# Kernel tuning notes

Hardware: AMD Instinct MI355X
Metric: run time of the kernel (lower is better)

Reference implementation:

```python
import jax, jax.numpy as jnp
import numpy as np

BUCKET_BINS = np.array([0, 1, 2, 3, 4, 5, 7, 8, 15, 16, 31, 32, 63, 64], dtype=np.int32)
MAX_WINDOW = 8  # args.span_maximum_length


def _span_index_table(L):
    # Static enumeration of all spans of width 1..MAX_WINDOW (stride-1 unfold).
    starts, ends = [], []
    for w in range(1, min(L, MAX_WINDOW) + 1):
        s = np.arange(0, L - w + 1)
        starts.append(s)
        ends.append(s + w)
    return (np.concatenate(starts).astype(np.int32),
            np.concatenate(ends).astype(np.int32))


def _bucket(width):
    # index of last bin with width >= bin value
    return jnp.searchsorted(jnp.asarray(BUCKET_BINS), width, side='right') - 1


def _fnn(h, W1, b1, W2, b2, W3, b3):
    # Linear->ReLU->(Dropout: eval identity)->Linear->ReLU->Linear->Softmax
    h = jax.nn.relu(h @ W1 + b1)
    h = jax.nn.relu(h @ W2 + b2)
    return jax.nn.softmax(h @ W3 + b3, axis=-1)


def setup_inputs() -> dict:
    key = jax.random.key(0)
    ks = jax.random.split(key, 16)
    B, L, D = 8, 256, 768
    H, WD, DD = 1024, 25, 25
    span_dim = 2 * D + WD          # 1561
    pair_dim = 2 * span_dim + DD   # 3147
    f = jnp.float32

    def g(k, shape, scale):
        return jax.random.normal(k, shape, dtype=f) * scale

    return {
        'x': g(ks[0], (B, L, D), 1.0),
        'width_emb': g(ks[1], (len(BUCKET_BINS), WD), 0.02),
        'dist_emb': g(ks[2], (len(BUCKET_BINS), DD), 0.02),
        'Ws1': g(ks[3], (span_dim, H), 0.02), 'bs1': jnp.zeros((H,), f),
        'Ws2': g(ks[4], (H, H), 0.02), 'bs2': jnp.zeros((H,), f),
        'Ws3': g(ks[5], (H, 3), 0.02), 'bs3': jnp.zeros((3,), f),
        'Wp1': g(ks[6], (pair_dim, H), 0.02), 'bp1': jnp.zeros((H,), f),
        'Wp2': g(ks[7], (H, H), 0.02), 'bp2': jnp.zeros((H,), f),
        'Wp3': g(ks[8], (H, 4), 0.02), 'bp3': jnp.zeros((4,), f),
        'nz': 64,
    }


def reference(x, width_emb, dist_emb, Ws1, bs1, Ws2, bs2, Ws3, bs3,
              Wp1, bp1, Wp2, bp2, Wp3, bp3, nz):
    B, L, D = x.shape
    starts_np, ends_np = _span_index_table(L)
    starts = jnp.asarray(starts_np)
    ends = jnp.asarray(ends_np)

    # ---- SpanRepresentation: [start token, end token, width bucket emb] ----
    w_emb = width_emb[_bucket(ends - starts)]                     # [S, WD]
    spans = jnp.concatenate([
        x[:, starts_np, :],                                       # [B,S,D]
        x[:, ends_np - 1, :],                                     # [B,S,D]
        jnp.broadcast_to(w_emb, (B,) + w_emb.shape),              # [B,S,WD]
    ], axis=-1)                                                   # [B,S,span_dim]

    # ---- span_fnn + PrunedTargetOpinion (top-k on aspect/opinion probs) ----
    span_prob = _fnn(spans, Ws1, bs1, Ws2, bs2, Ws3, bs3)         # [B,S,3]
    _, t_idx = jax.lax.top_k(span_prob[:, :, 1], nz)              # aspect  [B,nz]
    _, o_idx = jax.lax.top_k(span_prob[:, :, 2], nz)              # opinion [B,nz]

    # ---- PairRepresentation: all target x opinion pairs ----
    t_rep = jnp.take_along_axis(spans, t_idx[:, :, None], axis=1) # [B,nz,sd]
    o_rep = jnp.take_along_axis(spans, o_idx[:, :, None], axis=1)
    ta, tb = starts[t_idx], ends[t_idx]                           # [B,nz]
    oc, od = starts[o_idx], ends[o_idx]
    # min_distance(a,b,c,d) = min(|b-c|, |a-d|)
    dist = jnp.minimum(jnp.abs(tb[:, :, None] - oc[:, None, :]),
                       jnp.abs(ta[:, :, None] - od[:, None, :]))  # [B,nz,nz]
    d_emb = dist_emb[_bucket(dist)]                               # [B,nz,nz,DD]
    sd = spans.shape[-1]
    pairs = jnp.concatenate([
        jnp.broadcast_to(t_rep[:, :, None, :], (B, nz, nz, sd)),
        jnp.broadcast_to(o_rep[:, None, :, :], (B, nz, nz, sd)),
        d_emb,
    ], axis=-1).reshape(B, nz * nz, 2 * sd + d_emb.shape[-1])     # [B,nz^2,pair_dim]

    pair_prob = _fnn(pairs, Wp1, bp1, Wp2, bp2, Wp3, bp3)         # [B,nz^2,4]
    return span_prob, pair_prob
```

## Files before the change

kernel.cpp:

```cpp
#include <hip/hip_runtime.h>
#include <cstdint>
#include <cstddef>

#define BATCH 8
#define SEQ   256
#define DIM   768
#define NSPAN 2020
#define HID   1024
#define NZ    64

typedef unsigned short u16;
typedef unsigned int   u32;
typedef unsigned long long u64;

typedef __bf16 bf16x8 __attribute__((ext_vector_type(8)));
typedef float  f32x4  __attribute__((ext_vector_type(4)));

__device__ __forceinline__ u16 f2bf(float f) {
    union { float f; u32 u; } x; x.f = f;
    u32 r = x.u + 0x7fffu + ((x.u >> 16) & 1u);
    return (u16)(r >> 16);
}
__device__ __forceinline__ float bf2f(u16 b) {
    union { u32 u; float f; } x; x.u = ((u32)b) << 16;
    return x.f;
}
__device__ __forceinline__ void splitbf(float v, u16& h, u16& l) {
    h = f2bf(v);
    l = f2bf(v - bf2f(h));
}

__device__ __forceinline__ void gld_lds16(const void* g, void* l) {
    __builtin_amdgcn_global_load_lds(
        (const __attribute__((address_space(1))) unsigned int*)g,
        (__attribute__((address_space(3))) unsigned int*)l, 16, 0, 0);
}

__device__ __forceinline__ void span_decode(int s, int& start, int& end, int& w) {
    int off = 0;
#pragma unroll
    for (int wi = 1; wi <= 8; ++wi) {
        int cnt = SEQ - wi + 1;
        if (s < off + cnt) { w = wi; start = s - off; end = start + wi; return; }
        off += cnt;
    }
    w = 8; start = 0; end = 8;
}

__device__ __forceinline__ int dbucket(int d) {
    int b = 0;
    b += (d >= 1);  b += (d >= 2);  b += (d >= 3);  b += (d >= 4);
    b += (d >= 5);  b += (d >= 7);  b += (d >= 8);  b += (d >= 15);
    b += (d >= 16); b += (d >= 31); b += (d >= 32); b += (d >= 63);
    b += (d >= 64);
    return b;
}

__device__ __forceinline__ void xcd_map(int L, int sft, int& bx, int& by) {
    int grp = L >> (3 + sft);
    int rem = L & ((1 << (3 + sft)) - 1);
    bx = rem >> 3;
    by = (grp << 3) | (rem & 7);
}

__global__ __launch_bounds__(256) void k_prep(
    const float* __restrict__ x,  u16* __restrict__ xh,   u16* __restrict__ xl,
    const float* __restrict__ wemb, const float* __restrict__ demb,
    const float* __restrict__ bs1, const float* __restrict__ bp1,
    float* __restrict__ wtabS, float* __restrict__ wtabPt,
    float* __restrict__ wtabPo, float* __restrict__ dtab,
    const float* __restrict__ Ws1, u16* __restrict__ W1Th, u16* __restrict__ W1Tl,
    const float* __restrict__ Ws2, u16* __restrict__ W2Th, u16* __restrict__ W2Tl,
    const float* __restrict__ Wp2, u16* __restrict__ Wp2T,
    const float* __restrict__ Wp1, u16* __restrict__ Wp1T4)
{
    __shared__ float tile[32][33];
    const int bid = blockIdx.x, tid = threadIdx.x;
    if (bid < 6144) {
        int i = bid * 256 + tid;
        u16 h, l; splitbf(x[i], h, l);
        xh[i] = h; xl[i] = l;
        return;
    }
    if (bid < 6296) {
        int t = bid - 6144;
        int row = t >> 2;
        int h = (t & 3) * 256 + tid;
        const int wb[8] = {1,2,3,4,5,5,6,7};
        if (row < 8) {
            int bk = wb[row];
            float acc = bs1[h];
            for (int j = 0; j < 25; ++j) acc = fmaf(wemb[bk*25+j], Ws1[(size_t)(1536+j)*HID + h], acc);
            wtabS[row*HID + h] = acc;
        } else if (row < 16) {
            int bk = wb[row-8];
            float acc = 0.f;
            for (int j = 0; j < 25; ++j) acc = fmaf(wemb[bk*25+j], Wp1[(size_t)(1536+j)*HID + h], acc);
            wtabPt[(row-8)*HID + h] = acc;
        } else if (row < 24) {
            int bk = wb[row-16];
            float acc = 0.f;
            for (int j = 0; j < 25; ++j) acc = fmaf(wemb[bk*25+j], Wp1[(size_t)(3097+j)*HID + h], acc);
            wtabPo[(row-16)*HID + h] = acc;
        } else {
            int tt = row - 24;
            float acc = bp1[h];
            for (int j = 0; j < 25; ++j) acc = fmaf(demb[tt*25+j], Wp1[(size_t)(3122+j)*HID + h], acc);
            dtab[tt*HID + h] = acc;
        }
        return;
    }
    const int tb = bid - 6296;
    const int tr = tid >> 3;
    const int tc4 = (tid & 7) * 4;
    int job, tk, tn, blk = 0;
    if (tb < 1536)      { job = 0; tk = tb % 24; tn = tb / 24; }
    else if (tb < 2560) { job = 1; int t = tb - 1536; tk = t & 31; tn = t >> 5; }
    else if (tb < 3584) { job = 2; int t = tb - 2560; tk = t & 31; tn = t >> 5; }
    else                { job = 3; int t = tb - 3584; blk = t / 768; int r = t - blk * 768; tk = r % 24; tn = r / 24; }
    const int k0 = tk * 32, n0 = tn * 32;

    int k = k0 + tr;
    float4 v;
    if (job == 0) {
        const float* s = (n0 < 1024) ? (Ws1 + (size_t)k * HID + n0)
                                     : (Ws1 + (size_t)(768 + k) * HID + (n0 - 1024));
        v = *(const float4*)(s + tc4);
    } else if (job == 1) {
        v = *(const float4*)(Ws2 + (size_t)k * HID + n0 + tc4);
    } else if (job == 2) {
        v = *(const float4*)(Wp2 + (size_t)k * HID + n0 + tc4);
    } else {
        const int roff[4] = {0, 768, 1561, 2329};
        v = *(const float4*)(Wp1 + (size_t)(roff[blk] + k) * HID + n0 + tc4);
    }
    tile[tr][tc4+0] = v.x; tile[tr][tc4+1] = v.y;
    tile[tr][tc4+2] = v.z; tile[tr][tc4+3] = v.w;
    __syncthreads();

    int nn = n0 + tr;
    float w0 = tile[tc4+0][tr], w1 = tile[tc4+1][tr];
    float w2 = tile[tc4+2][tr], w3 = tile[tc4+3][tr];
    if (job == 0) {
        size_t d = (size_t)nn * 768 + k0 + tc4;
        u16 h0,l0,h1,l1,h2,l2,h3,l3;
        splitbf(w0,h0,l0); splitbf(w1,h1,l1); splitbf(w2,h2,l2); splitbf(w3,h3,l3);
        *(uint2*)(W1Th + d) = make_uint2((u32)h0 | ((u32)h1 << 16), (u32)h2 | ((u32)h3 << 16));
        *(uint2*)(W1Tl + d) = make_uint2((u32)l0 | ((u32)l1 << 16), (u32)l2 | ((u32)l3 << 16));
    } else if (job == 1) {
        size_t d = (size_t)nn * 1024 + k0 + tc4;
        u16 h0,l0,h1,l1,h2,l2,h3,l3;
        splitbf(w0,h0,l0); splitbf(w1,h1,l1); splitbf(w2,h2,l2); splitbf(w3,h3,l3);
        *(uint2*)(W2Th + d) = make_uint2((u32)h0 | ((u32)h1 << 16), (u32)h2 | ((u32)h3 << 16));
        *(uint2*)(W2Tl + d) = make_uint2((u32)l0 | ((u32)l1 << 16), (u32)l2 | ((u32)l3 << 16));
    } else if (job == 2) {
        size_t d = (size_t)nn * 1024 + k0 + tc4;
        *(uint2*)(Wp2T + d) = make_uint2((u32)f2bf(w0) | ((u32)f2bf(w1) << 16),
                                         (u32)f2bf(w2) | ((u32)f2bf(w3) << 16));
    } else {
        size_t d = (size_t)blk * 786432 + (size_t)nn * 768 + k0 + tc4;
        *(uint2*)(Wp1T4 + d) = make_uint2((u32)f2bf(w0) | ((u32)f2bf(w1) << 16),
                                          (u32)f2bf(w2) | ((u32)f2bf(w3) << 16));
    }
}

__global__ __launch_bounds__(256) void k_gemm3bf(
    const u16* __restrict__ Ah, const u16* __restrict__ Al, int lda,
    const u16* __restrict__ BTh, const u16* __restrict__ BTl, int ldb,
    float* __restrict__ C, int ldc,
    int M, int K, int nby, int sft)
{
    int bx, by;
    xcd_map(blockIdx.x, sft, bx, by);
    if (by >= nby) return;
    __shared__ __align__(16) u16 sm[4 * 128 * 32];
    u16* sAh = sm;
    u16* sAl = sm + 4096;
    u16* sBh = sm + 8192;
    u16* sBl = sm + 12288;
    const int tid = threadIdx.x;
    const int bm = by * 128, bn = bx * 128;
    const int wave = tid >> 6, lane = tid & 63;
    const int wr = wave >> 1, wc = wave & 1;
    const int q = lane >> 4, tl = lane & 15;

    f32x4 zero = {0.f, 0.f, 0.f, 0.f};
    f32x4 acc[4][4];
#pragma unroll
    for (int i = 0; i < 4; ++i)
#pragma unroll
        for (int j = 0; j < 4; ++j) acc[i][j] = zero;

    const int srow = lane >> 2;
    const int scol = (lane & 3) * 8;
    int ra0 = bm + wave * 32 + srow;      if (ra0 >= M) ra0 = M - 1;
    int ra1 = bm + wave * 32 + 16 + srow; if (ra1 >= M) ra1 = M - 1;
    const int rb0 = bn + wave * 32 + srow;
    const int rb1 = bn + wave * 32 + 16 + srow;
    u16* dA0 = sAh + wave * 1024;  u16* dA1 = dA0 + 512;
    u16* dL0 = sAl + wave * 1024;  u16* dL1 = dL0 + 512;
    u16* dB0 = sBh + wave * 1024;  u16* dB1 = dB0 + 512;
    u16* dC0 = sBl + wave * 1024;  u16* dC1 = dC0 + 512;
    const u16* gA0 = Ah  + (size_t)ra0 * lda + scol;
    const u16* gA1 = Ah  + (size_t)ra1 * lda + scol;
    const u16* gL0 = Al  + (size_t)ra0 * lda + scol;
    const u16* gL1 = Al  + (size_t)ra1 * lda + scol;
    const u16* gB0 = BTh + (size_t)rb0 * ldb + scol;
    const u16* gB1 = BTh + (size_t)rb1 * ldb + scol;
    const u16* gC0 = BTl + (size_t)rb0 * ldb + scol;
    const u16* gC1 = BTl + (size_t)rb1 * ldb + scol;

    for (int k0 = 0; k0 < K; k0 += 32) {
        gld_lds16(gA0 + k0, dA0);
        gld_lds16(gA1 + k0, dA1);
        gld_lds16(gL0 + k0, dL0);
        gld_lds16(gL1 + k0, dL1);
        gld_lds16(gB0 + k0, dB0);
        gld_lds16(gB1 + k0, dB1);
        gld_lds16(gC0 + k0, dC0);
        gld_lds16(gC1 + k0, dC1);
        __syncthreads();
        bf16x8 ah[4], al[4], bh[4], bl[4];
#pragma unroll
        for (int t = 0; t < 4; ++t) {
            int arow = (wr*64 + t*16 + tl) * 32 + q*8;
            int brow = (wc*64 + t*16 + tl) * 32 + q*8;
            ah[t] = *(const bf16x8*)(&sAh[arow]);
            al[t] = *(const bf16x8*)(&sAl[arow]);
            bh[t] = *(const bf16x8*)(&sBh[brow]);
            bl[t] = *(const bf16x8*)(&sBl[brow]);
        }
#pragma unroll
        for (int ti = 0; ti < 4; ++ti)
#pragma unroll
            for (int tj = 0; tj < 4; ++tj) {
                acc[ti][tj] = __builtin_amdgcn_mfma_f32_16x16x32_bf16(ah[ti], bh[tj], acc[ti][tj], 0, 0, 0);
                acc[ti][tj] = __builtin_amdgcn_mfma_f32_16x16x32_bf16(al[ti], bh[tj], acc[ti][tj], 0, 0, 0);
                acc[ti][tj] = __builtin_amdgcn_mfma_f32_16x16x32_bf16(ah[ti], bl[tj], acc[ti][tj], 0, 0, 0);
            }
        __syncthreads();
    }
#pragma unroll
    for (int ti = 0; ti < 4; ++ti) {
#pragma unroll
        for (int tj = 0; tj < 4; ++tj) {
            int gcol = bn + wc*64 + tj*16 + tl;
#pragma unroll
            for (int r = 0; r < 4; ++r) {
                int grow = bm + wr*64 + ti*16 + q*4 + r;
                if (grow >= M) continue;
                C[(size_t)grow * ldc + gcol] = acc[ti][tj][r];
            }
        }
    }
}

#define MFB __builtin_amdgcn_mfma_f32_16x16x32_bf16
#define MFROW(i, A, B) \
    acc[i][0] = MFB(A, B[0], acc[i][0], 0, 0, 0); \
    acc[i][1] = MFB(A, B[1], acc[i][1], 0, 0, 0); \
    acc[i][2] = MFB(A, B[2], acc[i][2], 0, 0, 0); \
    acc[i][3] = MFB(A, B[3], acc[i][3], 0, 0, 0);

__global__ __launch_bounds__(512, 2) void k_span_l2(
    const u16* __restrict__ Ah, const u16* __restrict__ Al,
    const u16* __restrict__ BTh, const u16* __restrict__ BTl,
    const float* __restrict__ bs2, const float* __restrict__ Ws3,
    float* __restrict__ part, int M)
{
    __shared__ __align__(16) u16 sm[65536];
    const int tid = threadIdx.x;
    const int swz = (blockIdx.x & 7) * 32 + (blockIdx.x >> 3);
    const int by = swz >> 2, bx = swz & 3;
    const int bm = by * 256, bn = bx * 256;
    const int wave = tid >> 6, lane = tid & 63;
    const int wm = wave >> 2, wn = wave & 3;
    const int tl = lane & 15, q8 = lane >> 4;

    const int sr  = lane >> 2;
    const int scs = lane & 3;
    const int scl = scs ^ ((sr >> 1) & 3);
    const u16* gsrc[8];
    u32 ldst[8];
#pragma unroll
    for (int c = 0; c < 4; ++c) {
        int arr  = 2 + (c >> 1);
        int half = c & 1;
        int sb   = wave;
        int row  = bn + half * 128 + sb * 16 + sr;
        const u16* base = (arr == 2) ? BTh : BTl;
        gsrc[c] = base + (size_t)row * HID + scl * 8;
        ldst[c] = arr * 8192 + half * 4096 + sb * 512;
    }
#pragma unroll
    for (int p = 0; p < 4; ++p) {
        int arr  = wave >> 2;
        int half = (wave >> 1) & 1;
        int sb   = 2 * p + (wave & 1);
        int row  = bm + half * 128 + sb * 16 + sr;
        if (row >= M) row = M - 1;
        const u16* base = arr ? Al : Ah;
        gsrc[4 + p] = base + (size_t)row * HID + scl * 8;
        ldst[4 + p] = arr * 8192 + half * 4096 + sb * 512;
    }
    const int cpr = q8 ^ ((tl >> 1) & 3);
    const u32 lof = (u32)(tl * 32 + cpr * 8);
    const u32 rA  = (u32)(wm * 4096) + lof;
    const u32 rB  = 16384u + (u32)((wn >> 1) * 4096 + (wn & 1) * 2048) + lof;

    f32x4 zero = {0.f, 0.f, 0.f, 0.f};
    f32x4 acc[8][4];
#pragma unroll
    for (int i = 0; i < 8; ++i)
#pragma unroll
        for (int j = 0; j < 4; ++j) acc[i][j] = zero;

#pragma unroll
    for (int c = 0; c < 8; ++c) gld_lds16(gsrc[c], sm + ldst[c]);
    asm volatile("s_waitcnt vmcnt(3)" ::: "memory");
    asm volatile("s_barrier" ::: "memory");

    bf16x8 bh[4], bl[4];
    bf16x8 aXh0, aXh1, aXl0, aXl1, aYh0, aYh1, aYl0, aYl1;
#pragma unroll
    for (int fn = 0; fn < 4; ++fn) {
        bh[fn] = *(const bf16x8*)(sm + rB + fn * 512);
        bl[fn] = *(const bf16x8*)(sm + rB + 8192 + fn * 512);
    }
    aXh0 = *(const bf16x8*)(sm + rA + 0 * 512);
    aXh1 = *(const bf16x8*)(sm + rA + 1 * 512);
    aXl0 = *(const bf16x8*)(sm + rA + 8192 + 0 * 512);
    aXl1 = *(const bf16x8*)(sm + rA + 8192 + 1 * 512);

    for (int t = 0; t < 32; ++t) {
        const u16* smr = sm + ((t & 1) ? 32768u : 0u);
        u16*       smw = sm + ((t & 1) ? 0u : 32768u);
        const int  kn  = (t + 1) * 32;
        gld_lds16(gsrc[0] + kn, smw + ldst[0]);
        gld_lds16(gsrc[1] + kn, smw + ldst[1]);
        gld_lds16(gsrc[2] + kn, smw + ldst[2]);
        asm volatile("s_waitcnt vmcnt(5)" ::: "memory");
        asm volatile("s_barrier" ::: "memory");
        __builtin_amdgcn_sched_barrier(0);
        __builtin_amdgcn_s_setprio(1);
        MFROW(0, aXh0, bh) MFROW(1, aXh1, bh)
        MFROW(0, aXl0, bh) MFROW(1, aXl1, bh)
        MFROW(0, aXh0, bl) MFROW(1, aXh1, bl)
        __builtin_amdgcn_s_setprio(0);
        __builtin_amdgcn_sched_barrier(0);
        aYh0 = *(const bf16x8*)(smr + rA + 2 * 512);
        aYh1 = *(const bf16x8*)(smr + rA + 3 * 512);
        aYl0 = *(const bf16x8*)(smr + rA + 8192 + 2 * 512);
        aYl1 = *(const bf16x8*)(smr + rA + 8192 + 3 * 512);
        gld_lds16(gsrc[3] + kn, smw + ldst[3]);
        gld_lds16(gsrc[4] + kn, smw + ldst[4]);
        asm volatile("s_waitcnt vmcnt(6)" ::: "memory");
        asm volatile("s_barrier" ::: "memory");
        __builtin_amdgcn_sched_barrier(0);
        __builtin_amdgcn_s_setprio(1);
        MFROW(2, aYh0, bh) MFROW(3, aYh1, bh)
        MFROW(2, aYl0, bh) MFROW(3, aYl1, bh)
        MFROW(2, aYh0, bl) MFROW(3, aYh1, bl)
        __builtin_amdgcn_s_setprio(0);
        __builtin_amdgcn_sched_barrier(0);
        aXh0 = *(const bf16x8*)(smr + rA + 4 * 512);
        aXh1 = *(const bf16x8*)(smr + rA + 5 * 512);
        aXl0 = *(const bf16x8*)(smr + rA + 8192 + 4 * 512);
        aXl1 = *(const bf16x8*)(smr + rA + 8192 + 5 * 512);
        gld_lds16(gsrc[5] + kn, smw + ldst[5]);
        gld_lds16(gsrc[6] + kn, smw + ldst[6]);
        asm volatile("s_waitcnt vmcnt(7)" ::: "memory");
        asm volatile("s_barrier" ::: "memory");
        __builtin_amdgcn_sched_barrier(0);
        __builtin_amdgcn_s_setprio(1);
        MFROW(4, aXh0, bh) MFROW(5, aXh1, bh)
        MFROW(4, aXl0, bh) MFROW(5, aXl1, bh)
        MFROW(4, aXh0, bl) MFROW(5, aXh1, bl)
        __builtin_amdgcn_s_setprio(0);
        __builtin_amdgcn_sched_barrier(0);
        aYh0 = *(const bf16x8*)(smr + rA + 6 * 512);
        aYh1 = *(const bf16x8*)(smr + rA + 7 * 512);
        aYl0 = *(const bf16x8*)(smr + rA + 8192 + 6 * 512);
        aYl1 = *(const bf16x8*)(smr + rA + 8192 + 7 * 512);
        gld_lds16(gsrc[7] + kn, smw + ldst[7]);
        asm volatile("s_waitcnt vmcnt(3)" ::: "memory");
        asm volatile("s_barrier" ::: "memory");
        __builtin_amdgcn_sched_barrier(0);
        __builtin_amdgcn_s_setprio(1);
        MFROW(6, aYh0, bh) MFROW(7, aYh1, bh)
        MFROW(6, aYl0, bh) MFROW(7, aYl1, bh)
        MFROW(6, aYh0, bl) MFROW(7, aYh1, bl)
        __builtin_amdgcn_s_setprio(0);
        __builtin_amdgcn_sched_barrier(0);
        aXh0 = *(const bf16x8*)(smw + rA + 0 * 512);
        aXh1 = *(const bf16x8*)(smw + rA + 1 * 512);
        aXl0 = *(const bf16x8*)(smw + rA + 8192 + 0 * 512);
        aXl1 = *(const bf16x8*)(smw + rA + 8192 + 1 * 512);
#pragma unroll
        for (int fn = 0; fn < 4; ++fn) {
            bh[fn] = *(const bf16x8*)(smw + rB + fn * 512);
            bl[fn] = *(const bf16x8*)(smw + rB + 8192 + fn * 512);
        }
        asm volatile("s_barrier" ::: "memory");
    }

    const int slot = bx * 4 + wn;
#pragma unroll
    for (int fm = 0; fm < 8; ++fm) {
#pragma unroll
        for (int r = 0; r < 4; ++r) {
            int grow = bm + wm * 128 + fm * 16 + q8 * 4 + r;
            float l0 = 0.f, l1 = 0.f, l2 = 0.f;
#pragma unroll
            for (int fn = 0; fn < 4; ++fn) {
                int gcol = bn + wn * 64 + fn * 16 + tl;
                float v = fmaxf(acc[fm][fn][r] + bs2[gcol], 0.f);
                const float* w3 = Ws3 + gcol * 3;
                l0 = fmaf(v, w3[0], l0);
                l1 = fmaf(v, w3[1], l1);
                l2 = fmaf(v, w3[2], l2);
            }
#pragma unroll
            for (int off = 8; off > 0; off >>= 1) {
                l0 += __shfl_down(l0, off, 16);
                l1 += __shfl_down(l1, off, 16);
                l2 += __shfl_down(l2, off, 16);
            }
            if (tl == 0 && grow < M) {
                float* dst = part + ((size_t)grow * 16 + slot) * 3;
                dst[0] = l0; dst[1] = l1; dst[2] = l2;
            }
        }
    }
    asm volatile("s_waitcnt vmcnt(0)" ::: "memory");
}

__global__ __launch_bounds__(256) void k_pairL1(
    const u16* __restrict__ xh, const u16* __restrict__ Wp1T4,
    float* __restrict__ TO2, const int* __restrict__ toks)
{
    __shared__ __align__(16) u16 sm[2 * 64 * 32];
    u16* sA = sm;
    u16* sB = sm + 2048;
    const int tid = threadIdx.x;
    const int bid = blockIdx.x;
    const int p = bid >> 8;
    const int bx = bid & 15, by = (bid >> 4) & 15;
    const int bm = by * 64, bn = bx * 64;
    const int wave = tid >> 6, lane = tid & 63;
    const int wr = wave >> 1, wc = wave & 1;
    const int q = lane >> 4, tl = lane & 15;
    const bool isO = bm >= 512;

    f32x4 zero = {0.f, 0.f, 0.f, 0.f};
    f32x4 acc[2][2];
#pragma unroll
    for (int i = 0; i < 2; ++i)
#pragma unroll
        for (int j = 0; j < 2; ++j) acc[i][j] = zero;

    const int srow = tid >> 2;
    const int scol = (tid & 3) * 8;
    u16* dA = sA + wave * 512;
    u16* dB = sB + wave * 512;

    int arow = toks[bm + srow + p * 1024];
    const u16* gA = xh + (size_t)arow * DIM + scol;
    const u16* gB = Wp1T4 + ((size_t)((isO ? 2 : 0) + p) * 1024 + bn + srow) * DIM + scol;
    for (int k0 = 0; k0 < DIM; k0 += 32) {
        gld_lds16(gA + k0, dA);
        gld_lds16(gB + k0, dB);
        __syncthreads();
        bf16x8 af[2], bf[2];
#pragma unroll
        for (int t = 0; t < 2; ++t) {
            af[t] = *(const bf16x8*)(&sA[(wr*32 + t*16 + tl) * 32 + q*8]);
            bf[t] = *(const bf16x8*)(&sB[(wc*32 + t*16 + tl) * 32 + q*8]);
        }
#pragma unroll
        for (int ti = 0; ti < 2; ++ti)
#pragma unroll
            for (int tj = 0; tj < 2; ++tj)
                acc[ti][tj] = __builtin_amdgcn_mfma_f32_16x16x32_bf16(af[ti], bf[tj], acc[ti][tj], 0, 0, 0);
        __syncthreads();
    }
    float* dstb = TO2 + (size_t)p * 1024 * HID;
#pragma unroll
    for (int ti = 0; ti < 2; ++ti) {
#pragma unroll
        for (int tj = 0; tj < 2; ++tj) {
            int gcol = bn + wc*32 + tj*16 + tl;
#pragma unroll
            for (int r = 0; r < 4; ++r) {
                int grow = bm + wr*32 + ti*16 + q*4 + r;
                dstb[(size_t)grow * HID + gcol] = acc[ti][tj][r];
            }
        }
    }
}

__global__ __launch_bounds__(256) void k_build_h1s(
    const float* __restrict__ XALL, const float* __restrict__ wtabS,
    u16* __restrict__ h1h, u16* __restrict__ h1l)
{
    int r = blockIdx.x;
    int b = r / NSPAN, s = r - b * NSPAN;
    int st, en, w; span_decode(s, st, en, w);
    const float4* xs = (const float4*)(XALL + (size_t)(b*SEQ + st) * 2048);
    const float4* xe = (const float4*)(XALL + (size_t)(b*SEQ + en - 1) * 2048 + 1024);
    const float4* wt = (const float4*)(wtabS + (size_t)(w-1) * HID);
    int t = threadIdx.x;
    float4 a = xs[t], bz = xe[t], c = wt[t];
    float v0 = fmaxf(a.x + bz.x + c.x, 0.f);
    float v1 = fmaxf(a.y + bz.y + c.y, 0.f);
    float v2 = fmaxf(a.z + bz.z + c.z, 0.f);
    float v3 = fmaxf(a.w + bz.w + c.w, 0.f);
    u16 h0,l0,h1,l1,h2,l2,h3,l3;
    splitbf(v0,h0,l0); splitbf(v1,h1,l1); splitbf(v2,h2,l2); splitbf(v3,h3,l3);
    size_t base = (size_t)r * HID + t * 4;
    *(uint2*)(h1h + base) = make_uint2((u32)h0 | ((u32)h1 << 16), (u32)h2 | ((u32)h3 << 16));
    *(uint2*)(h1l + base) = make_uint2((u32)l0 | ((u32)l1 << 16), (u32)l2 | ((u32)l3 << 16));
}

__global__ __launch_bounds__(1024) void k_topk(
    const float* __restrict__ partS, const float* __restrict__ bs3,
    float* __restrict__ out, int* __restrict__ t_idx, int* __restrict__ o_idx,
    int* __restrict__ toks)
{
    int b = blockIdx.x >> 1;
    int head = 1 + (blockIdx.x & 1);
    int* outp = (head == 1 ? t_idx : o_idx) + b * NZ;
    __shared__ u64 keys[2048];
    int tid = threadIdx.x;
#pragma unroll
    for (int ii = 0; ii < 2; ++ii) {
        int s = tid + ii * 1024;
        u32 fb = 0;
        if (s < NSPAN) {
            const float* p = partS + (size_t)(b * NSPAN + s) * 48;
            float s0 = bs3[0], s1 = bs3[1], s2 = bs3[2];
#pragma unroll
            for (int t = 0; t < 16; ++t) {
                s0 += p[t*3]; s1 += p[t*3+1]; s2 += p[t*3+2];
            }
            float m = fmaxf(s0, fmaxf(s1, s2));
            float e0 = expf(s0 - m), e1 = expf(s1 - m), e2 = expf(s2 - m);
            float inv = 1.f / (e0 + e1 + e2);
            float p0 = e0 * inv, p1 = e1 * inv, p2 = e2 * inv;
            float* o = out + (size_t)(b * NSPAN + s) * 3;
            o[0] = p0; o[1] = p1; o[2] = p2;
            union { float f; u32 u; } x;
            x.f = (head == 1) ? p1 : p2;
            fb = x.u;
        }
        keys[s] = ((u64)fb << 32) | (u64)(0xFFFFFFFFu - (u32)s);
    }
    __syncthreads();
    for (int k = 2; k <= 2048; k <<= 1) {
        for (int j = k >> 1; j > 0; j >>= 1) {
#pragma unroll
            for (int ii = 0; ii < 2; ++ii) {
                int i = tid + ii * 1024;
                int ixj = i ^ j;
                if (ixj > i) {
                    u64 a = keys[i], c = keys[ixj];
                    bool desc = (i & k) == 0;
                    bool wrong = desc ? (a < c) : (a > c);
                    if (wrong) { keys[i] = c; keys[ixj] = a; }
                }
            }
            __syncthreads();
        }
    }
    if (tid < NZ) {
        u64 key = keys[tid];
        int fi = (int)(0xFFFFFFFFu - (u32)(key & 0xFFFFFFFFu));
        if (fi < 0 || fi >= NSPAN) fi = 0;
        outp[tid] = fi;
        int st, en, w; span_decode(fi, st, en, w);
        int base = (head == 1 ? 0 : 512) + b * NZ + tid;
        toks[base] = b * SEQ + st;
        toks[1024 + base] = b * SEQ + en - 1;
    }
}

__global__ __launch_bounds__(256) void k_build_h1p(
    const float* __restrict__ TO2, const int* __restrict__ t_idx, const int* __restrict__ o_idx,
    const float* __restrict__ wtabPt, const float* __restrict__ wtabPo,
    const float* __restrict__ dtab, u16* __restrict__ h1p)
{
    __shared__ float Ts[8][HID];
    __shared__ float Os[4][HID];
    const int bid = blockIdx.x;
    const int b = bid >> 7;
    const int it = (bid >> 4) & 7;
    const int jt = bid & 15;
    const int i0 = it * 8, j0 = jt * 4;
    const int tid = threadIdx.x;
    const int k4 = tid * 4;
    const size_t PS = (size_t)1024 * HID;

    int tinfo[8][2];
    int oinfo[4][2];
#pragma unroll
    for (int r = 0; r < 8; ++r) {
        int i = i0 + r;
        int ts = t_idx[b*64 + i];
        int ta, tb, wt; span_decode(ts, ta, tb, wt);
        tinfo[r][0] = ta; tinfo[r][1] = tb;
        float4 t0 = *(const float4*)(TO2 + (size_t)(b*64 + i) * HID + k4);
        float4 t1 = *(const float4*)(TO2 + PS + (size_t)(b*64 + i) * HID + k4);
        float4 pp = *(const float4*)(wtabPt + (size_t)(wt-1) * HID + k4);
        Ts[r][k4+0] = t0.x + t1.x + pp.x;
        Ts[r][k4+1] = t0.y + t1.y + pp.y;
        Ts[r][k4+2] = t0.z + t1.z + pp.z;
        Ts[r][k4+3] = t0.w + t1.w + pp.w;
    }
#pragma unroll
    for (int r = 0; r < 4; ++r) {
        int j = j0 + r;
        int os = o_idx[b*64 + j];
        int oc, od, wo; span_decode(os, oc, od, wo);
        oinfo[r][0] = oc; oinfo[r][1] = od;
        float4 o0 = *(const float4*)(TO2 + (size_t)(512 + b*64 + j) * HID + k4);
        float4 o1 = *(const float4*)(TO2 + PS + (size_t)(512 + b*64 + j) * HID + k4);
        float4 qq = *(const float4*)(wtabPo + (size_t)(wo-1) * HID + k4);
        Os[r][k4+0] = o0.x + o1.x + qq.x;
        Os[r][k4+1] = o0.y + o1.y + qq.y;
        Os[r][k4+2] = o0.z + o1.z + qq.z;
        Os[r][k4+3] = o0.w + o1.w + qq.w;
    }
    __syncthreads();

#pragma unroll
    for (int ri = 0; ri < 8; ++ri) {
#pragma unroll
        for (int rj = 0; rj < 4; ++rj) {
            int ta = tinfo[ri][0], tb = tinfo[ri][1];
            int oc = oinfo[rj][0], od = oinfo[rj][1];
            int d1 = tb - oc; d1 = d1 < 0 ? -d1 : d1;
            int d2 = ta - od; d2 = d2 < 0 ? -d2 : d2;
            int dist = d1 < d2 ? d1 : d2;
            int db = dbucket(dist);
            const float4 dd = *(const float4*)(dtab + (size_t)db * HID + k4);
            float vx = fmaxf(Ts[ri][k4+0] + Os[rj][k4+0] + dd.x, 0.f);
            float vy = fmaxf(Ts[ri][k4+1] + Os[rj][k4+1] + dd.y, 0.f);
            float vz = fmaxf(Ts[ri][k4+2] + Os[rj][k4+2] + dd.z, 0.f);
            float vw = fmaxf(Ts[ri][k4+3] + Os[rj][k4+3] + dd.w, 0.f);
            u32 p0 = (u32)f2bf(vx) | ((u32)f2bf(vy) << 16);
            u32 p1 = (u32)f2bf(vz) | ((u32)f2bf(vw) << 16);
            int row = b * 4096 + (i0 + ri) * 64 + (j0 + rj);
            *(uint2*)(h1p + (size_t)row * HID + k4) = make_uint2(p0, p1);
        }
    }
}

#define MFROWP(i, A0, A1, B0, B1) \
    acc[i][0] = MFB(A0, B0[0], acc[i][0], 0, 0, 0); \
    acc[i][1] = MFB(A0, B0[1], acc[i][1], 0, 0, 0); \
    acc[i][2] = MFB(A0, B0[2], acc[i][2], 0, 0, 0); \
    acc[i][3] = MFB(A0, B0[3], acc[i][3], 0, 0, 0);

__global__ __launch_bounds__(512, 2) void k_pair_l2(
    const u16* __restrict__ Abf, const u16* __restrict__ BT,
    const float* __restrict__ bp2, const float* __restrict__ Wp3,
    float* __restrict__ part)
{
    __shared__ __align__(16) u16 sm[65536];
    const int tid = threadIdx.x;
    const int swz = (blockIdx.x & 7) * 64 + (blockIdx.x >> 3);
    const int by = swz >> 2, bx = swz & 3;
    const int bm = by * 256, bn = bx * 256;
    const int wave = tid >> 6, lane = tid & 63;
    const int wm = wave >> 2, wn = wave & 3;
    const int tl = lane & 15, q8 = lane >> 4;

    const int sr  = lane >> 2;
    const int scs = lane & 3;
    const int scl = scs ^ ((sr >> 1) & 3);
    const u16* gsrc[8];
    u32 ldst[8];
#pragma unroll
    for (int c = 0; c < 4; ++c) {
        int half = c >> 1;
        int sb   = (c & 1) * 8 + wave;
        int row  = bn + half * 128 + (sb >> 1) * 16 + sr;
        gsrc[c] = BT + (size_t)row * HID + (sb & 1) * 32 + scl * 8;
        ldst[c] = 16384 + half * 8192 + sb * 512;
    }
#pragma unroll
    for (int p = 0; p < 4; ++p) {
        int half = wave >> 2;
        int sb   = 4 * p + (wave & 3);
        int row  = bm + half * 128 + (sb >> 1) * 16 + sr;
        gsrc[4 + p] = Abf + (size_t)row * HID + (sb & 1) * 32 + scl * 8;
        ldst[4 + p] = half * 8192 + sb * 512;
    }
    const int cpr = q8 ^ ((tl >> 1) & 3);
    const u32 lof = (u32)(tl * 32 + cpr * 8);
    const u32 rA  = (u32)(wm * 8192) + lof;
    const u32 rB  = 16384u + (u32)((wn >> 1) * 8192 + (wn & 1) * 4096) + lof;

    f32x4 zero = {0.f, 0.f, 0.f, 0.f};
    f32x4 acc[8][4];
#pragma unroll
    for (int i = 0; i < 8; ++i)
#pragma unroll
        for (int j = 0; j < 4; ++j) acc[i][j] = zero;

#pragma unroll
    for (int c = 0; c < 8; ++c) gld_lds16(gsrc[c], sm + ldst[c]);
    asm volatile("s_waitcnt vmcnt(3)" ::: "memory");
    asm volatile("s_barrier" ::: "memory");

    bf16x8 b0[4], b1[4];
    bf16x8 xa00, xa01, xa10, xa11, ya00, ya01, ya10, ya11;
#pragma unroll
    for (int fn = 0; fn < 4; ++fn) {
        b0[fn] = *(const bf16x8*)(sm + rB + (fn * 2 + 0) * 512);
        b1[fn] = *(const bf16x8*)(sm + rB + (fn * 2 + 1) * 512);
    }
    xa00 = *(const bf16x8*)(sm + rA + 0 * 512);
    xa01 = *(const bf16x8*)(sm + rA + 1 * 512);
    xa10 = *(const bf16x8*)(sm + rA + 2 * 512);
    xa11 = *(const bf16x8*)(sm + rA + 3 * 512);

    for (int t = 0; t < 16; ++t) {
        const u16* smr = sm + ((t & 1) ? 32768u : 0u);
        u16*       smw = sm + ((t & 1) ? 0u : 32768u);
        const int  kn  = (t + 1) * 64;
        gld_lds16(gsrc[0] + kn, smw + ldst[0]);
        gld_lds16(gsrc[1] + kn, smw + ldst[1]);
        gld_lds16(gsrc[2] + kn, smw + ldst[2]);
        asm volatile("s_waitcnt vmcnt(5)" ::: "memory");
        asm volatile("s_barrier" ::: "memory");
        __builtin_amdgcn_sched_barrier(0);
        __builtin_amdgcn_s_setprio(1);
        MFROW(0, xa00, b0) MFROW(1, xa10, b0)
        MFROW(0, xa01, b1) MFROW(1, xa11, b1)
        __builtin_amdgcn_s_setprio(0);
        __builtin_amdgcn_sched_barrier(0);
        ya00 = *(const bf16x8*)(smr + rA + 4 * 512);
        ya01 = *(const bf16x8*)(smr + rA + 5 * 512);
        ya10 = *(const bf16x8*)(smr + rA + 6 * 512);
        ya11 = *(const bf16x8*)(smr + rA + 7 * 512);
        gld_lds16(gsrc[3] + kn, smw + ldst[3]);
        gld_lds16(gsrc[4] + kn, smw + ldst[4]);
        asm volatile("s_waitcnt vmcnt(6)" ::: "memory");
        asm volatile("s_barrier" ::: "memory");
        __builtin_amdgcn_sched_barrier(0);
        __builtin_amdgcn_s_setprio(1);
        MFROW(2, ya00, b0) MFROW(3, ya10, b0)
        MFROW(2, ya01, b1) MFROW(3, ya11, b1)
        __builtin_amdgcn_s_setprio(0);
        __builtin_amdgcn_sched_barrier(0);
        xa00 = *(const bf16x8*)(smr + rA + 8 * 512);
        xa01 = *(const bf16x8*)(smr + rA + 9 * 512);
        xa10 = *(const bf16x8*)(smr + rA + 10 * 512);
        xa11 = *(const bf16x8*)(smr + rA + 11 * 512);
        gld_lds16(gsrc[5] + kn, smw + ldst[5]);
        gld_lds16(gsrc[6] + kn, smw + ldst[6]);
        asm volatile("s_waitcnt vmcnt(7)" ::: "memory");
        asm volatile("s_barrier" ::: "memory");
        __builtin_amdgcn_sched_barrier(0);
        __builtin_amdgcn_s_setprio(1);
        MFROW(4, xa00, b0) MFROW(5, xa10, b0)
        MFROW(4, xa01, b1) MFROW(5, xa11, b1)
        __builtin_amdgcn_s_setprio(0);
        __builtin_amdgcn_sched_barrier(0);
        ya00 = *(const bf16x8*)(smr + rA + 12 * 512);
        ya01 = *(const bf16x8*)(smr + rA + 13 * 512);
        ya10 = *(const bf16x8*)(smr + rA + 14 * 512);
        ya11 = *(const bf16x8*)(smr + rA + 15 * 512);
        gld_lds16(gsrc[7] + kn, smw + ldst[7]);
        asm volatile("s_waitcnt vmcnt(3)" ::: "memory");
        asm volatile("s_barrier" ::: "memory");
        __builtin_amdgcn_sched_barrier(0);
        __builtin_amdgcn_s_setprio(1);
        MFROW(6, ya00, b0) MFROW(7, ya10, b0)
        MFROW(6, ya01, b1) MFROW(7, ya11, b1)
        __builtin_amdgcn_s_setprio(0);
        __builtin_amdgcn_sched_barrier(0);
        xa00 = *(const bf16x8*)(smw + rA + 0 * 512);
        xa01 = *(const bf16x8*)(smw + rA + 1 * 512);
        xa10 = *(const bf16x8*)(smw + rA + 2 * 512);
        xa11 = *(const bf16x8*)(smw + rA + 3 * 512);
#pragma unroll
        for (int fn = 0; fn < 4; ++fn) {
            b0[fn] = *(const bf16x8*)(smw + rB + (fn * 2 + 0) * 512);
            b1[fn] = *(const bf16x8*)(smw + rB + (fn * 2 + 1) * 512);
        }
        asm volatile("s_barrier" ::: "memory");
    }

    const int slot = bx * 4 + wn;
#pragma unroll
    for (int fm = 0; fm < 8; ++fm) {
#pragma unroll
        for (int r = 0; r < 4; ++r) {
            int grow = bm + wm * 128 + fm * 16 + q8 * 4 + r;
            float l0 = 0.f, l1 = 0.f, l2 = 0.f, l3 = 0.f;
#pragma unroll
            for (int fn = 0; fn < 4; ++fn) {
                int gcol = bn + wn * 64 + fn * 16 + tl;
                float v = fmaxf(acc[fm][fn][r] + bp2[gcol], 0.f);
                const float4 w = *(const float4*)(Wp3 + gcol * 4);
                l0 = fmaf(v, w.x, l0); l1 = fmaf(v, w.y, l1);
                l2 = fmaf(v, w.z, l2); l3 = fmaf(v, w.w, l3);
            }
#pragma unroll
            for (int off = 8; off > 0; off >>= 1) {
                l0 += __shfl_down(l0, off, 16);
                l1 += __shfl_down(l1, off, 16);
                l2 += __shfl_down(l2, off, 16);
                l3 += __shfl_down(l3, off, 16);
            }
            if (tl == 0) {
                float* dst = part + ((size_t)grow * 16 + slot) * 4;
                dst[0] = l0; dst[1] = l1; dst[2] = l2; dst[3] = l3;
            }
        }
    }
    asm volatile("s_waitcnt vmcnt(0)" ::: "memory");
}

__global__ __launch_bounds__(256) void k_pair_red(
    const float* __restrict__ part, const float* __restrict__ bp3,
    float* __restrict__ out)
{
    int r = blockIdx.x * 256 + threadIdx.x;
    const float4* p = (const float4*)(part + (size_t)r * 64);
    float s0 = bp3[0], s1 = bp3[1], s2 = bp3[2], s3 = bp3[3];
#pragma unroll
    for (int t = 0; t < 16; ++t) {
        float4 v = p[t];
        s0 += v.x; s1 += v.y; s2 += v.z; s3 += v.w;
    }
    float m = fmaxf(fmaxf(s0, s1), fmaxf(s2, s3));
    float e0 = expf(s0 - m), e1 = expf(s1 - m), e2 = expf(s2 - m), e3 = expf(s3 - m);
    float inv = 1.f / (e0 + e1 + e2 + e3);
    float* o = out + (size_t)r * 4;
    o[0] = e0 * inv; o[1] = e1 * inv; o[2] = e2 * inv; o[3] = e3 * inv;
}

extern "C" void kernel_launch(void* const* d_in, const int* in_sizes, int n_in,
                              void* d_out, int out_size, void* d_ws, size_t ws_size,
                              hipStream_t stream)
{
    const float* x    = (const float*)d_in[0];
    const float* wemb = (const float*)d_in[1];
    const float* demb = (const float*)d_in[2];
    const float* Ws1  = (const float*)d_in[3];
    const float* bs1  = (const float*)d_in[4];
    const float* Ws2  = (const float*)d_in[5];
    const float* bs2  = (const float*)d_in[6];
    const float* Ws3  = (const float*)d_in[7];
    const float* bs3  = (const float*)d_in[8];
    const float* Wp1  = (const float*)d_in[9];
    const float* bp1  = (const float*)d_in[10];
    const float* Wp2  = (const float*)d_in[11];
    const float* bp2  = (const float*)d_in[12];
    const float* Wp3  = (const float*)d_in[13];
    const float* bp3  = (const float*)d_in[14];
    float* out = (float*)d_out;
    char* ws = (char*)d_ws;

    const size_t RSZ = (size_t)32768 * HID * 2;
    size_t off = 0;
    auto alloc = [&](size_t bytes) -> void* {
        void* p = ws + off;
        off += (bytes + 255) & ~(size_t)255;
        return p;
    };
    char* R1 = (char*)alloc(RSZ);
    char* R2 = (char*)alloc(RSZ);
    u16*   h1h  = (u16*)R1;
    u16*   h1l  = (u16*)(R1 + (size_t)16160 * HID * 2);
    float* XALL = (float*)R2;
    u16*   xl   = (u16*)(R2 + (16u << 20));
    u16*   W1Th = (u16*)(R2 + (19u << 20));
    u16*   W1Tl = (u16*)(R2 + (22u << 20));
    u16*   h1p  = (u16*)R2;
    u16*   xh     = (u16*)alloc((size_t)2048 * DIM * 2);
    float* TO2    = (float*)alloc((size_t)2 * 1024 * HID * 4);
    float* partS  = (float*)alloc((size_t)16160 * 16 * 3 * 4);
    float* partP  = (float*)alloc((size_t)32768 * 16 * 4 * 4);
    u16*   W2Th   = (u16*)alloc((size_t)1024 * 1024 * 2);
    u16*   W2Tl   = (u16*)alloc((size_t)1024 * 1024 * 2);
    u16*   Wp2T   = (u16*)alloc((size_t)1024 * 1024 * 2);
    u16*   Wp1T4  = (u16*)alloc((size_t)4 * 1024 * 768 * 2);
    float* wtabS  = (float*)alloc(8 * HID * 4);
    float* wtabPt = (float*)alloc(8 * HID * 4);
    float* wtabPo = (float*)alloc(8 * HID * 4);
    float* dtab   = (float*)alloc(14 * HID * 4);
    int*   t_idx  = (int*)alloc(BATCH * NZ * 4);
    int*   o_idx  = (int*)alloc(BATCH * NZ * 4);
    int*   toks   = (int*)alloc(2048 * 4);
    (void)ws_size; (void)in_sizes; (void)n_in; (void)out_size;

    k_prep<<<12952, 256, 0, stream>>>(x, xh, xl, wemb, demb, bs1, bp1,
                                      wtabS, wtabPt, wtabPo, dtab,
                                      Ws1, W1Th, W1Tl, Ws2, W2Th, W2Tl,
                                      Wp2, Wp2T, Wp1, Wp1T4);

    k_gemm3bf<<<256, 256, 0, stream>>>(xh, xl, 768, W1Th, W1Tl, 768,
                                       XALL, 2048, 2048, 768, 16, 4);
    k_build_h1s<<<16160, 256, 0, stream>>>(XALL, wtabS, h1h, h1l);
    k_span_l2<<<256, 512, 0, stream>>>(h1h, h1l, W2Th, W2Tl, bs2, Ws3, partS, 16160);
    k_topk<<<16, 1024, 0, stream>>>(partS, bs3, out, t_idx, o_idx, toks);
    k_pairL1<<<512, 256, 0, stream>>>(xh, Wp1T4, TO2, toks);
    k_build_h1p<<<1024, 256, 0, stream>>>(TO2, t_idx, o_idx, wtabPt, wtabPo, dtab, h1p);
    k_pair_l2<<<512, 512, 0, stream>>>(h1p, Wp2T, bp2, Wp3, partP);
    k_pair_red<<<128, 256, 0, stream>>>(partP, bp3, out + 48480);
}
```

Measured before the change: 410.5 us.

## Double-buffer LDS in span and pair-L1 GEMMs; interleave LDS reads with MFMAs

```diff
diff --git a/kernel.cpp b/kernel.cpp
--- a/kernel.cpp
+++ b/kernel.cpp
@@ -173,11 +173,7 @@
     int bx, by;
     xcd_map(blockIdx.x, sft, bx, by);
     if (by >= nby) return;
-    __shared__ __align__(16) u16 sm[4 * 128 * 32];
-    u16* sAh = sm;
-    u16* sAl = sm + 4096;
-    u16* sBh = sm + 8192;
-    u16* sBl = sm + 12288;
+    __shared__ __align__(16) u16 sm[2 * 16384];
     const int tid = threadIdx.x;
     const int bm = by * 128, bn = bx * 128;
     const int wave = tid >> 6, lane = tid & 63;
@@ -197,10 +193,10 @@
     int ra1 = bm + wave * 32 + 16 + srow; if (ra1 >= M) ra1 = M - 1;
     const int rb0 = bn + wave * 32 + srow;
     const int rb1 = bn + wave * 32 + 16 + srow;
-    u16* dA0 = sAh + wave * 1024;  u16* dA1 = dA0 + 512;
-    u16* dL0 = sAl + wave * 1024;  u16* dL1 = dL0 + 512;
-    u16* dB0 = sBh + wave * 1024;  u16* dB1 = dB0 + 512;
-    u16* dC0 = sBl + wave * 1024;  u16* dC1 = dC0 + 512;
+    const u32 oA0 = wave * 1024,          oA1 = oA0 + 512;
+    const u32 oL0 = 4096 + wave * 1024,   oL1 = oL0 + 512;
+    const u32 oB0 = 8192 + wave * 1024,   oB1 = oB0 + 512;
+    const u32 oC0 = 12288 + wave * 1024,  oC1 = oC0 + 512;
     const u16* gA0 = Ah  + (size_t)ra0 * lda + scol;
     const u16* gA1 = Ah  + (size_t)ra1 * lda + scol;
     const u16* gL0 = Al  + (size_t)ra0 * lda + scol;
@@ -210,25 +206,37 @@
     const u16* gC0 = BTl + (size_t)rb0 * ldb + scol;
     const u16* gC1 = BTl + (size_t)rb1 * ldb + scol;
 
-    for (int k0 = 0; k0 < K; k0 += 32) {
-        gld_lds16(gA0 + k0, dA0);
-        gld_lds16(gA1 + k0, dA1);
-        gld_lds16(gL0 + k0, dL0);
-        gld_lds16(gL1 + k0, dL1);
-        gld_lds16(gB0 + k0, dB0);
-        gld_lds16(gB1 + k0, dB1);
-        gld_lds16(gC0 + k0, dC0);
-        gld_lds16(gC1 + k0, dC1);
-        __syncthreads();
+    gld_lds16(gA0, sm + oA0); gld_lds16(gA1, sm + oA1);
+    gld_lds16(gL0, sm + oL0); gld_lds16(gL1, sm + oL1);
+    gld_lds16(gB0, sm + oB0); gld_lds16(gB1, sm + oB1);
+    gld_lds16(gC0, sm + oC0); gld_lds16(gC1, sm + oC1);
+    asm volatile("s_waitcnt vmcnt(0)" ::: "memory");
+    asm volatile("s_barrier" ::: "memory");
+
+    const int NT = K >> 5;
+    for (int kt = 0; kt < NT; ++kt) {
+        const u16* smr = sm + ((kt & 1) ? 16384u : 0u);
+        u16*       smw = sm + ((kt & 1) ? 0u : 16384u);
+        if (kt < NT - 1) {
+            const int k0 = (kt + 1) * 32;
+            gld_lds16(gA0 + k0, smw + oA0); gld_lds16(gA1 + k0, smw + oA1);
+            gld_lds16(gL0 + k0, smw + oL0); gld_lds16(gL1 + k0, smw + oL1);
+            gld_lds16(gB0 + k0, smw + oB0); gld_lds16(gB1 + k0, smw + oB1);
+            gld_lds16(gC0 + k0, smw + oC0); gld_lds16(gC1 + k0, smw + oC1);
+            asm volatile("s_waitcnt vmcnt(8)" ::: "memory");
+        } else {
+            asm volatile("s_waitcnt vmcnt(0)" ::: "memory");
+        }
+        asm volatile("s_barrier" ::: "memory");
         bf16x8 ah[4], al[4], bh[4], bl[4];
 #pragma unroll
         for (int t = 0; t < 4; ++t) {
             int arow = (wr*64 + t*16 + tl) * 32 + q*8;
             int brow = (wc*64 + t*16 + tl) * 32 + q*8;
-            ah[t] = *(const bf16x8*)(&sAh[arow]);
-            al[t] = *(const bf16x8*)(&sAl[arow]);
-            bh[t] = *(const bf16x8*)(&sBh[brow]);
-            bl[t] = *(const bf16x8*)(&sBl[brow]);
+            ah[t] = *(const bf16x8*)(smr + arow);
+            al[t] = *(const bf16x8*)(smr + 4096 + arow);
+            bh[t] = *(const bf16x8*)(smr + 8192 + brow);
+            bl[t] = *(const bf16x8*)(smr + 12288 + brow);
         }
 #pragma unroll
         for (int ti = 0; ti < 4; ++ti)
@@ -238,7 +246,7 @@
                 acc[ti][tj] = __builtin_amdgcn_mfma_f32_16x16x32_bf16(al[ti], bh[tj], acc[ti][tj], 0, 0, 0);
                 acc[ti][tj] = __builtin_amdgcn_mfma_f32_16x16x32_bf16(ah[ti], bl[tj], acc[ti][tj], 0, 0, 0);
             }
-        __syncthreads();
+        asm volatile("s_barrier" ::: "memory");
     }
 #pragma unroll
     for (int ti = 0; ti < 4; ++ti) {
@@ -344,14 +352,13 @@
         __builtin_amdgcn_sched_barrier(0);
         __builtin_amdgcn_s_setprio(1);
         MFROW(0, aXh0, bh) MFROW(1, aXh1, bh)
-        MFROW(0, aXl0, bh) MFROW(1, aXl1, bh)
-        MFROW(0, aXh0, bl) MFROW(1, aXh1, bl)
-        __builtin_amdgcn_s_setprio(0);
-        __builtin_amdgcn_sched_barrier(0);
         aYh0 = *(const bf16x8*)(smr + rA + 2 * 512);
         aYh1 = *(const bf16x8*)(smr + rA + 3 * 512);
         aYl0 = *(const bf16x8*)(smr + rA + 8192 + 2 * 512);
         aYl1 = *(const bf16x8*)(smr + rA + 8192 + 3 * 512);
+        MFROW(0, aXl0, bh) MFROW(1, aXl1, bh)
+        MFROW(0, aXh0, bl) MFROW(1, aXh1, bl)
+        __builtin_amdgcn_s_setprio(0);
         gld_lds16(gsrc[3] + kn, smw + ldst[3]);
         gld_lds16(gsrc[4] + kn, smw + ldst[4]);
         asm volatile("s_waitcnt vmcnt(6)" ::: "memory");
@@ -359,14 +366,13 @@
         __builtin_amdgcn_sched_barrier(0);
         __builtin_amdgcn_s_setprio(1);
         MFROW(2, aYh0, bh) MFROW(3, aYh1, bh)
-        MFROW(2, aYl0, bh) MFROW(3, aYl1, bh)
-        MFROW(2, aYh0, bl) MFROW(3, aYh1, bl)
-        __builtin_amdgcn_s_setprio(0);
-        __builtin_amdgcn_sched_barrier(0);
         aXh0 = *(const bf16x8*)(smr + rA + 4 * 512);
         aXh1 = *(const bf16x8*)(smr + rA + 5 * 512);
         aXl0 = *(const bf16x8*)(smr + rA + 8192 + 4 * 512);
         aXl1 = *(const bf16x8*)(smr + rA + 8192 + 5 * 512);
+        MFROW(2, aYl0, bh) MFROW(3, aYl1, bh)
+        MFROW(2, aYh0, bl) MFROW(3, aYh1, bl)
+        __builtin_amdgcn_s_setprio(0);
         gld_lds16(gsrc[5] + kn, smw + ldst[5]);
         gld_lds16(gsrc[6] + kn, smw + ldst[6]);
         asm volatile("s_waitcnt vmcnt(7)" ::: "memory");
@@ -374,28 +380,26 @@
         __builtin_amdgcn_sched_barrier(0);
         __builtin_amdgcn_s_setprio(1);
         MFROW(4, aXh0, bh) MFROW(5, aXh1, bh)
-        MFROW(4, aXl0, bh) MFROW(5, aXl1, bh)
-        MFROW(4, aXh0, bl) MFROW(5, aXh1, bl)
-        __builtin_amdgcn_s_setprio(0);
-        __builtin_amdgcn_sched_barrier(0);
         aYh0 = *(const bf16x8*)(smr + rA + 6 * 512);
         aYh1 = *(const bf16x8*)(smr + rA + 7 * 512);
         aYl0 = *(const bf16x8*)(smr + rA + 8192 + 6 * 512);
         aYl1 = *(const bf16x8*)(smr + rA + 8192 + 7 * 512);
+        MFROW(4, aXl0, bh) MFROW(5, aXl1, bh)
+        MFROW(4, aXh0, bl) MFROW(5, aXh1, bl)
+        __builtin_amdgcn_s_setprio(0);
         gld_lds16(gsrc[7] + kn, smw + ldst[7]);
         asm volatile("s_waitcnt vmcnt(3)" ::: "memory");
         asm volatile("s_barrier" ::: "memory");
         __builtin_amdgcn_sched_barrier(0);
         __builtin_amdgcn_s_setprio(1);
         MFROW(6, aYh0, bh) MFROW(7, aYh1, bh)
-        MFROW(6, aYl0, bh) MFROW(7, aYl1, bh)
-        MFROW(6, aYh0, bl) MFROW(7, aYh1, bl)
-        __builtin_amdgcn_s_setprio(0);
-        __builtin_amdgcn_sched_barrier(0);
         aXh0 = *(const bf16x8*)(smw + rA + 0 * 512);
         aXh1 = *(const bf16x8*)(smw + rA + 1 * 512);
         aXl0 = *(const bf16x8*)(smw + rA + 8192 + 0 * 512);
         aXl1 = *(const bf16x8*)(smw + rA + 8192 + 1 * 512);
+        MFROW(6, aYl0, bh) MFROW(7, aYl1, bh)
+        MFROW(6, aYh0, bl) MFROW(7, aYh1, bl)
+        __builtin_amdgcn_s_setprio(0);
 #pragma unroll
         for (int fn = 0; fn < 4; ++fn) {
             bh[fn] = *(const bf16x8*)(smw + rB + fn * 512);
@@ -439,9 +443,7 @@
     const u16* __restrict__ xh, const u16* __restrict__ Wp1T4,
     float* __restrict__ TO2, const int* __restrict__ toks)
 {
-    __shared__ __align__(16) u16 sm[2 * 64 * 32];
-    u16* sA = sm;
-    u16* sB = sm + 2048;
+    __shared__ __align__(16) u16 sm[2 * 4096];
     const int tid = threadIdx.x;
     const int bid = blockIdx.x;
     const int p = bid >> 8;
@@ -461,28 +463,43 @@
 
     const int srow = tid >> 2;
     const int scol = (tid & 3) * 8;
-    u16* dA = sA + wave * 512;
-    u16* dB = sB + wave * 512;
+    const u32 oA = wave * 512;
+    const u32 oB = 2048 + wave * 512;
 
     int arow = toks[bm + srow + p * 1024];
     const u16* gA = xh + (size_t)arow * DIM + scol;
     const u16* gB = Wp1T4 + ((size_t)((isO ? 2 : 0) + p) * 1024 + bn + srow) * DIM + scol;
-    for (int k0 = 0; k0 < DIM; k0 += 32) {
-        gld_lds16(gA + k0, dA);
-        gld_lds16(gB + k0, dB);
-        __syncthreads();
+
+    gld_lds16(gA, sm + oA);
+    gld_lds16(gB, sm + oB);
+    asm volatile("s_waitcnt vmcnt(0)" ::: "memory");
+    asm volatile("s_barrier" ::: "memory");
+
+    const int NT = DIM / 32;
+    for (int kt = 0; kt < NT; ++kt) {
+        const u16* smr = sm + ((kt & 1) ? 4096u : 0u);
+        u16*       smw = sm + ((kt & 1) ? 0u : 4096u);
+        if (kt < NT - 1) {
+            const int k0 = (kt + 1) * 32;
+            gld_lds16(gA + k0, smw + oA);
+            gld_lds16(gB + k0, smw + oB);
+            asm volatile("s_waitcnt vmcnt(2)" ::: "memory");
+        } else {
+            asm volatile("s_waitcnt vmcnt(0)" ::: "memory");
+        }
+        asm volatile("s_barrier" ::: "memory");
         bf16x8 af[2], bf[2];
 #pragma unroll
         for (int t = 0; t < 2; ++t) {
-            af[t] = *(const bf16x8*)(&sA[(wr*32 + t*16 + tl) * 32 + q*8]);
-            bf[t] = *(const bf16x8*)(&sB[(wc*32 + t*16 + tl) * 32 + q*8]);
+            af[t] = *(const bf16x8*)(smr + (wr*32 + t*16 + tl) * 32 + q*8);
+            bf[t] = *(const bf16x8*)(smr + 2048 + (wc*32 + t*16 + tl) * 32 + q*8);
         }
 #pragma unroll
         for (int ti = 0; ti < 2; ++ti)
 #pragma unroll
             for (int tj = 0; tj < 2; ++tj)
                 acc[ti][tj] = __builtin_amdgcn_mfma_f32_16x16x32_bf16(af[ti], bf[tj], acc[ti][tj], 0, 0, 0);
-        __syncthreads();
+        asm volatile("s_barrier" ::: "memory");
     }
     float* dstb = TO2 + (size_t)p * 1024 * HID;
 #pragma unroll
@@ -655,12 +672,6 @@
     }
 }
 
-#define MFROWP(i, A0, A1, B0, B1) \
-    acc[i][0] = MFB(A0, B0[0], acc[i][0], 0, 0, 0); \
-    acc[i][1] = MFB(A0, B0[1], acc[i][1], 0, 0, 0); \
-    acc[i][2] = MFB(A0, B0[2], acc[i][2], 0, 0, 0); \
-    acc[i][3] = MFB(A0, B0[3], acc[i][3], 0, 0, 0);
-
 __global__ __launch_bounds__(512, 2) void k_pair_l2(
     const u16* __restrict__ Abf, const u16* __restrict__ BT,
     const float* __restrict__ bp2, const float* __restrict__ Wp3,
@@ -737,13 +748,12 @@
         __builtin_amdgcn_sched_barrier(0);
         __builtin_amdgcn_s_setprio(1);
         MFROW(0, xa00, b0) MFROW(1, xa10, b0)
-        MFROW(0, xa01, b1) MFROW(1, xa11, b1)
-        __builtin_amdgcn_s_setprio(0);
-        __builtin_amdgcn_sched_barrier(0);
         ya00 = *(const bf16x8*)(smr + rA + 4 * 512);
         ya01 = *(const bf16x8*)(smr + rA + 5 * 512);
         ya10 = *(const bf16x8*)(smr + rA + 6 * 512);
         ya11 = *(const bf16x8*)(smr + rA + 7 * 512);
+        MFROW(0, xa01, b1) MFROW(1, xa11, b1)
+        __builtin_amdgcn_s_setprio(0);
         gld_lds16(gsrc[3] + kn, smw + ldst[3]);
         gld_lds16(gsrc[4] + kn, smw + ldst[4]);
         asm volatile("s_waitcnt vmcnt(6)" ::: "memory");
@@ -751,13 +761,12 @@
         __builtin_amdgcn_sched_barrier(0);
         __builtin_amdgcn_s_setprio(1);
         MFROW(2, ya00, b0) MFROW(3, ya10, b0)
-        MFROW(2, ya01, b1) MFROW(3, ya11, b1)
-        __builtin_amdgcn_s_setprio(0);
-        __builtin_amdgcn_sched_barrier(0);
         xa00 = *(const bf16x8*)(smr + rA + 8 * 512);
         xa01 = *(const bf16x8*)(smr + rA + 9 * 512);
         xa10 = *(const bf16x8*)(smr + rA + 10 * 512);
         xa11 = *(const bf16x8*)(smr + rA + 11 * 512);
+        MFROW(2, ya01, b1) MFROW(3, ya11, b1)
+        __builtin_amdgcn_s_setprio(0);
         gld_lds16(gsrc[5] + kn, smw + ldst[5]);
         gld_lds16(gsrc[6] + kn, smw + ldst[6]);
         asm volatile("s_waitcnt vmcnt(7)" ::: "memory");
@@ -765,26 +774,24 @@
         __builtin_amdgcn_sched_barrier(0);
         __builtin_amdgcn_s_setprio(1);
         MFROW(4, xa00, b0) MFROW(5, xa10, b0)
-        MFROW(4, xa01, b1) MFROW(5, xa11, b1)
-        __builtin_amdgcn_s_setprio(0);
-        __builtin_amdgcn_sched_barrier(0);
         ya00 = *(const bf16x8*)(smr + rA + 12 * 512);
         ya01 = *(const bf16x8*)(smr + rA + 13 * 512);
         ya10 = *(const bf16x8*)(smr + rA + 14 * 512);
         ya11 = *(const bf16x8*)(smr + rA + 15 * 512);
+        MFROW(4, xa01, b1) MFROW(5, xa11, b1)
+        __builtin_amdgcn_s_setprio(0);
         gld_lds16(gsrc[7] + kn, smw + ldst[7]);
         asm volatile("s_waitcnt vmcnt(3)" ::: "memory");
         asm volatile("s_barrier" ::: "memory");
         __builtin_amdgcn_sched_barrier(0);
         __builtin_amdgcn_s_setprio(1);
         MFROW(6, ya00, b0) MFROW(7, ya10, b0)
-        MFROW(6, ya01, b1) MFROW(7, ya11, b1)
-        __builtin_amdgcn_s_setprio(0);
-        __builtin_amdgcn_sched_barrier(0);
         xa00 = *(const bf16x8*)(smw + rA + 0 * 512);
         xa01 = *(const bf16x8*)(smw + rA + 1 * 512);
         xa10 = *(const bf16x8*)(smw + rA + 2 * 512);
         xa11 = *(const bf16x8*)(smw + rA + 3 * 512);
+        MFROW(6, ya01, b1) MFROW(7, ya11, b1)
+        __builtin_amdgcn_s_setprio(0);
 #pragma unroll
         for (int fn = 0; fn < 4; ++fn) {
             b0[fn] = *(const bf16x8*)(smw + rB + (fn * 2 + 0) * 512);
```

Measured after the change: 457.6 us. 11.5% more time.
